# Kernel tuning notes

Hardware: AMD Instinct MI355X
Metric: run time of the kernel (lower is better)

The kernel has to match this reference:

```python
import jax, jax.numpy as jnp
import numpy as np

B, N, IN_DIM = 2, 512, 512
MEM, HID = 300, 64
NEG_SLOPE = 0.01


def setup_inputs() -> dict:
    key = jax.random.key(0)
    ks = jax.random.split(key, 10)
    feature = jax.random.normal(ks[0], (B, N, IN_DIM), dtype=jnp.float32)
    adj = jax.random.randint(ks[1], (B, N, N), 0, 2).astype(jnp.float32)
    s = 0.05
    # per-layer node projections W[l]
    w0 = jax.random.normal(ks[2], (IN_DIM, MEM), dtype=jnp.float32) * s
    b0 = jnp.zeros((MEM,), dtype=jnp.float32)
    w1 = jax.random.normal(ks[3], (MEM, MEM), dtype=jnp.float32) * s
    b1 = jnp.zeros((MEM,), dtype=jnp.float32)
    # shared attention MLP (afcs): Linear(2*MEM, HID) -> ReLU -> Linear(HID, 1)
    a1_w = jax.random.normal(ks[4], (2 * MEM, HID), dtype=jnp.float32) * s
    a1_b = jnp.zeros((HID,), dtype=jnp.float32)
    a2_w = jax.random.normal(ks[5], (HID, 1), dtype=jnp.float32) * s
    a2_b = jnp.zeros((1,), dtype=jnp.float32)
    return {"feature": feature, "adj": adj, "w0": w0, "b0": b0, "w1": w1,
            "b1": b1, "a1_w": a1_w, "a1_b": a1_b, "a2_w": a2_w, "a2_b": a2_b}


def _gat_layer(h_in, adj, w, b, a1_w, a1_b, a2_w, a2_b):
    h = h_in @ w + b                                   # (B,N,M)
    # cat([h_i, h_j]) @ a1_w split into the two halves (same math, no N^2*2M tensor)
    s_i = h @ a1_w[:MEM]                               # (B,N,H)
    s_j = h @ a1_w[MEM:]                               # (B,N,H)
    z = jax.nn.relu(s_i[:, :, None, :] + s_j[:, None, :, :] + a1_b)   # (B,N,N,H)
    e = (z @ a2_w)[..., 0] + a2_b[0]                   # (B,N,N)
    e = jax.nn.leaky_relu(e, negative_slope=NEG_SLOPE)
    b_, n_ = adj.shape[0], adj.shape[1]
    dmask = adj.reshape(b_, n_ * n_)
    logits = e.reshape(b_, n_ * n_) * dmask + (1.0 - dmask) * (-1e30)
    # NOTE: softmax over ALL N*N flattened edges (faithful to original dim=1)
    att = jax.nn.softmax(logits, axis=1).reshape(b_, n_, n_)
    return jnp.einsum('bij,bjd->bid', att, h)


def reference(feature, adj, w0, b0, w1, b1, a1_w, a1_b, a2_w, a2_b):
    f = _gat_layer(feature, adj, w0, b0, a1_w, a1_b, a2_w, a2_b)
    f = _gat_layer(f, adj, w1, b1, a1_w, a1_b, a2_w, a2_b)  # dropout = identity (eval)
    return f
```

## Files before the change

kernel.cpp:

```cpp
#include <hip/hip_runtime.h>

namespace {

constexpr int B_  = 2;
constexpr int N_  = 512;
constexpr int IN_ = 512;
constexpr int M_  = 300;
constexpr int H_  = 64;
constexpr float SLOPE_ = 0.01f;

constexpr long OFF_W0AI = 0;
constexpr long OFF_W0AJ = OFF_W0AI + 512L * 64;
constexpr long OFF_W1AI = OFF_W0AJ + 512L * 64;
constexpr long OFF_W1AJ = OFF_W1AI + 300L * 64;
constexpr long OFF_BSI0 = OFF_W1AJ + 300L * 64;
constexpr long OFF_BSJ0 = OFF_BSI0 + 64;
constexpr long OFF_BSI1 = OFF_BSJ0 + 64;
constexpr long OFF_BSJ1 = OFF_BSI1 + 64;
constexpr long OFF_H0   = OFF_BSJ1 + 64;
constexpr long OFF_H0P  = OFF_H0   + 307200;
constexpr long OFF_SI0P = OFF_H0P  + 2L * 307200;
constexpr long OFF_SJ0P = OFF_SI0P + 4L * 65536;
constexpr long OFF_F1P  = OFF_SJ0P + 4L * 65536;
constexpr long OFF_H1   = OFF_F1P  + 4L * 307200;
constexpr long OFF_H1P  = OFF_H1   + 307200;
constexpr long OFF_SI1P = OFF_H1P  + 2L * 307200;
constexpr long OFF_SJ1P = OFF_SI1P + 2L * 65536;
constexpr long OFF_ZP0  = OFF_SJ1P + 2L * 65536;
constexpr long OFF_ZP1  = OFF_ZP0  + 512;
constexpr long OFF_P0   = OFF_ZP1  + 512;
constexpr long OFF_P1   = OFF_P0   + 2L * 512 * 512;

__device__ __forceinline__ float4 f4add(float4 a, float4 b) {
    a.x += b.x; a.y += b.y; a.z += b.z; a.w += b.w; return a;
}

template<int AFOLD>
__device__ __forceinline__ void gemm_tile(
    const float* __restrict__ A, long afstride,
    const float* __restrict__ W, const float* __restrict__ bias,
    const float* __restrict__ Zp, float* __restrict__ C, long cslice,
    int K, int lda, int Cc, int R, int split, int local,
    float (*As)[38], float (*Ws)[64], float* zred)
{
    const int tx  = (Cc + 63) >> 6;
    const int ty  = (R + 31) >> 5;
    const int nrc = tx * ty;
    const int tile  = local % nrc;
    const int slice = local / nrc;
    const int row0 = (tile / tx) * 32;
    const int col0 = (tile % tx) * 64;
    const int nslab = (K + 31) >> 5;
    const int spl   = (nslab + split - 1) / split;
    const int kb    = slice * spl * 32;
    const int Ke    = min(K, kb + spl * 32);
    C += (long)slice * cslice;

    const int t   = threadIdx.x;
    const int ar  = t >> 3;
    const int ak  = (t & 7) * 4;
    const int arow = min(row0 + ar, R - 1);
    const int wk  = t >> 4;
    const int wc  = (t & 15) * 4;
    const int tm0 = (t >> 4) * 2;
    const int tn0 = (t & 15) * 4;

    auto loadA = [&](int k0) -> float4 {
        const int k = k0 + ak;
        const long base = (long)arow * lda + k;
        float4 r = make_float4(0.f, 0.f, 0.f, 0.f);
        if (k + 3 < Ke) {
            #pragma unroll
            for (int s = 0; s < AFOLD; ++s)
                r = f4add(r, *(const float4*)(A + (long)s * afstride + base));
        } else {
            #pragma unroll
            for (int u = 0; u < 4; ++u)
                if (k + u < Ke) {
                    float v = 0.f;
                    #pragma unroll
                    for (int s = 0; s < AFOLD; ++s)
                        v += A[(long)s * afstride + base + u];
                    (&r.x)[u] = v;
                }
        }
        return r;
    };
    auto loadW = [&](int k0, int s) -> float4 {
        const int gk = k0 + wk + 16 * s;
        if (gk < Ke) {
            const int c = col0 + wc;
            if (c + 3 < Cc) return *(const float4*)(W + (long)gk * Cc + c);
            float tv[4];
            #pragma unroll
            for (int u = 0; u < 4; ++u)
                tv[u] = (c + u < Cc) ? W[(long)gk * Cc + c + u] : 0.0f;
            return make_float4(tv[0], tv[1], tv[2], tv[3]);
        }
        return make_float4(0.f, 0.f, 0.f, 0.f);
    };

    float acc[2][4] = {};
    float4 av  = loadA(kb);
    float4 wv0 = loadW(kb, 0);
    float4 wv1 = loadW(kb, 1);

    for (int k0 = kb; k0 < Ke; k0 += 32) {
        As[ak + 0][ar] = av.x;
        As[ak + 1][ar] = av.y;
        As[ak + 2][ar] = av.z;
        As[ak + 3][ar] = av.w;
        *(float4*)&Ws[wk][wc]      = wv0;
        *(float4*)&Ws[wk + 16][wc] = wv1;
        __syncthreads();

        if (k0 + 32 < Ke) {
            av  = loadA(k0 + 32);
            wv0 = loadW(k0 + 32, 0);
            wv1 = loadW(k0 + 32, 1);
        }

        #pragma unroll
        for (int k = 0; k < 32; ++k) {
            const float a0 = As[k][tm0];
            const float a1 = As[k][tm0 + 1];
            const float4 w4 = *(const float4*)&Ws[k][tn0];
            acc[0][0] = fmaf(a0, w4.x, acc[0][0]);
            acc[0][1] = fmaf(a0, w4.y, acc[0][1]);
            acc[0][2] = fmaf(a0, w4.z, acc[0][2]);
            acc[0][3] = fmaf(a0, w4.w, acc[0][3]);
            acc[1][0] = fmaf(a1, w4.x, acc[1][0]);
            acc[1][1] = fmaf(a1, w4.y, acc[1][1]);
            acc[1][2] = fmaf(a1, w4.z, acc[1][2]);
            acc[1][3] = fmaf(a1, w4.w, acc[1][3]);
        }
        __syncthreads();
    }

    float scale = 1.0f;
    if (Zp != nullptr) {
        float v = Zp[t];
        #pragma unroll
        for (int off = 32; off > 0; off >>= 1)
            v += __shfl_down(v, off, 64);
        if ((t & 63) == 0) zred[t >> 6] = v;
        __syncthreads();
        scale = 1.0f / (zred[0] + zred[1] + zred[2] + zred[3]);
    }

    const int cbase = col0 + tn0;
    float bv[4] = {0.f, 0.f, 0.f, 0.f};
    if (bias != nullptr && slice == 0) {
        #pragma unroll
        for (int u = 0; u < 4; ++u)
            if (cbase + u < Cc) bv[u] = bias[cbase + u];
    }
    #pragma unroll
    for (int i = 0; i < 2; ++i) {
        const int r = row0 + tm0 + i;
        if (r < R) {
            if (cbase + 3 < Cc) {
                float4 o;
                o.x = fmaf(acc[i][0], scale, bv[0]);
                o.y = fmaf(acc[i][1], scale, bv[1]);
                o.z = fmaf(acc[i][2], scale, bv[2]);
                o.w = fmaf(acc[i][3], scale, bv[3]);
                *(float4*)(C + (long)r * Cc + cbase) = o;
            } else {
                #pragma unroll
                for (int u = 0; u < 4; ++u)
                    if (cbase + u < Cc)
                        C[(long)r * Cc + cbase + u] = fmaf(acc[i][u], scale, bv[u]);
            }
        }
    }
}

struct JobsK {
    const float* A[8]; long afstride[8];
    const float* W[8]; const float* bias[8]; const float* Zp[8];
    float* C[8]; long cslice[8];
    int K[8]; int lda[8]; int Cc[8]; int R[8]; int split[8];
    int off[8]; int njobs;
};

template<int AFOLD>
__global__ __launch_bounds__(256)
void gemm_jobs(JobsK jb)
{
    __shared__ __align__(16) float As[32][38];
    __shared__ __align__(16) float Ws[32][64];
    __shared__ float zred[4];

    const int bid = blockIdx.x;
    int j = jb.njobs - 1;
    while (j > 0 && bid < jb.off[j]) --j;
    const int local = bid - jb.off[j];

    gemm_tile<AFOLD>(jb.A[j], jb.afstride[j], jb.W[j], jb.bias[j], jb.Zp[j],
                     jb.C[j], jb.cslice[j], jb.K[j], jb.lda[j], jb.Cc[j],
                     jb.R[j], jb.split[j], local, As, Ws, zred);
}

template<int FOLD>
__device__ __forceinline__ void attn_tile(
    const float* __restrict__ si, const float* __restrict__ sj, long fstride,
    const float* __restrict__ adj, const float* __restrict__ a2w,
    const float* __restrict__ a2b, float* __restrict__ p,
    float* __restrict__ Zpart, int g,
    float (*Si)[68], float (*Sj)[68], float* red)
{
    const int b    = g >> 8;
    const int tile = g & 255;
    const int i0 = (tile >> 4) * 32;
    const int j0 = (tile & 15) * 32;
    const int t  = threadIdx.x;

    {
        const int r  = t >> 3;
        const int hc = (t & 7) * 8;
        const long gib = ((long)(b * N_ + i0 + r)) * H_ + hc;
        const long gjb = ((long)(b * N_ + j0 + r)) * H_ + hc;
        float4 a0 = make_float4(0.f, 0.f, 0.f, 0.f);
        float4 a1 = a0, b0v = a0, b1v = a0;
        #pragma unroll
        for (int s = 0; s < FOLD; ++s) {
            const float* gi = si + (long)s * fstride + gib;
            const float* gj = sj + (long)s * fstride + gjb;
            a0  = f4add(a0,  *(const float4*)(gi));
            a1  = f4add(a1,  *(const float4*)(gi + 4));
            b0v = f4add(b0v, *(const float4*)(gj));
            b1v = f4add(b1v, *(const float4*)(gj + 4));
        }
        *(float4*)&Si[r][hc]     = a0;
        *(float4*)&Si[r][hc + 4] = a1;
        *(float4*)&Sj[r][hc]     = b0v;
        *(float4*)&Sj[r][hc + 4] = b1v;
    }
    __syncthreads();

    const int i  = t >> 3;
    const int jl = t & 7;

    float e[4] = {0.f, 0.f, 0.f, 0.f};
    #pragma unroll
    for (int h0 = 0; h0 < H_; h0 += 4) {
        const float4 a4 = *(const float4*)&Si[i][h0];
        const float w0v = a2w[h0 + 0];
        const float w1v = a2w[h0 + 1];
        const float w2v = a2w[h0 + 2];
        const float w3v = a2w[h0 + 3];
        #pragma unroll
        for (int u = 0; u < 4; ++u) {
            const float4 b4 = *(const float4*)&Sj[jl + 8 * u][h0];
            e[u] = fmaf(fmaxf(a4.x + b4.x, 0.f), w0v, e[u]);
            e[u] = fmaf(fmaxf(a4.y + b4.y, 0.f), w1v, e[u]);
            e[u] = fmaf(fmaxf(a4.z + b4.z, 0.f), w2v, e[u]);
            e[u] = fmaf(fmaxf(a4.w + b4.w, 0.f), w3v, e[u]);
        }
    }

    const float a2bv = a2b[0];
    const long rowbase = ((long)(b * N_ + i0 + i)) * N_ + j0 + jl;
    float lsum = 0.f;
    #pragma unroll
    for (int u = 0; u < 4; ++u) {
        float ev = e[u] + a2bv;
        ev = (ev >= 0.f) ? ev : SLOPE_ * ev;
        const float m  = adj[rowbase + 8 * u];
        const float pv = m * __expf(ev);
        p[rowbase + 8 * u] = pv;
        lsum += pv;
    }

    #pragma unroll
    for (int off = 32; off > 0; off >>= 1)
        lsum += __shfl_down(lsum, off, 64);
    if ((t & 63) == 0) red[t >> 6] = lsum;
    __syncthreads();
    if (t == 0)
        Zpart[b * 256 + tile] = red[0] + red[1] + red[2] + red[3];
}

template<int FOLD>
__global__ __launch_bounds__(256)
void attn_fused(const float* __restrict__ si, const float* __restrict__ sj,
                const float* __restrict__ adj, const float* __restrict__ a2w,
                const float* __restrict__ a2b, float* __restrict__ p,
                float* __restrict__ Zpart,
                const float4* __restrict__ hsrc, float4* __restrict__ hdst)
{
    __shared__ __align__(16) float Si[32][68];
    __shared__ __align__(16) float Sj[32][68];
    __shared__ float red[4];

    const int bx = blockIdx.x;
    if (bx < 512) {
        attn_tile<FOLD>(si, sj, 65536, adj, a2w, a2b, p, Zpart, bx,
                        Si, Sj, red);
    } else {
        const int tid = (bx - 512) * 256 + threadIdx.x;
        for (int i = tid; i < 76800; i += 65536)
            hdst[i] = f4add(hsrc[i], hsrc[i + 76800]);
    }
}

}

extern "C" void kernel_launch(void* const* d_in, const int* in_sizes, int n_in,
                              void* d_out, int out_size, void* d_ws, size_t ws_size,
                              hipStream_t stream)
{
    (void)in_sizes; (void)n_in; (void)out_size; (void)ws_size;
    const float* feature = (const float*)d_in[0];
    const float* adj     = (const float*)d_in[1];
    const float* w0      = (const float*)d_in[2];
    const float* b0      = (const float*)d_in[3];
    const float* w1      = (const float*)d_in[4];
    const float* b1      = (const float*)d_in[5];
    const float* a1w     = (const float*)d_in[6];
    const float* a1b     = (const float*)d_in[7];
    const float* a2w     = (const float*)d_in[8];
    const float* a2b     = (const float*)d_in[9];
    float* out = (float*)d_out;
    float* ws  = (float*)d_ws;

    float* cW0Ai = ws + OFF_W0AI;
    float* cW0Aj = ws + OFF_W0AJ;
    float* cW1Ai = ws + OFF_W1AI;
    float* cW1Aj = ws + OFF_W1AJ;
    float* bsi0  = ws + OFF_BSI0;
    float* bsj0  = ws + OFF_BSJ0;
    float* bsi1  = ws + OFF_BSI1;
    float* bsj1  = ws + OFF_BSJ1;
    float* h0    = ws + OFF_H0;
    float* h0p   = ws + OFF_H0P;
    float* si0p  = ws + OFF_SI0P;
    float* sj0p  = ws + OFF_SJ0P;
    float* f1p   = ws + OFF_F1P;
    float* h1    = ws + OFF_H1;
    float* h1p   = ws + OFF_H1P;
    float* si1p  = ws + OFF_SI1P;
    float* sj1p  = ws + OFF_SJ1P;
    float* Zp0   = ws + OFF_ZP0;
    float* Zp1   = ws + OFF_ZP1;
    float* p0    = ws + OFF_P0;
    float* p1    = ws + OFF_P1;

    const float* Ai = a1w;
    const float* Aj = a1w + (long)M_ * H_;

    auto set_job = [](JobsK& jb, int j, const float* A, long afstride,
                      const float* W, const float* bias, const float* Zp,
                      float* C, long cslice, int K, int lda, int Cc, int R,
                      int split, int& tiles) {
        jb.A[j] = A; jb.afstride[j] = afstride;
        jb.W[j] = W; jb.bias[j] = bias; jb.Zp[j] = Zp;
        jb.C[j] = C; jb.cslice[j] = cslice;
        jb.K[j] = K; jb.lda[j] = lda; jb.Cc[j] = Cc; jb.R[j] = R;
        jb.split[j] = split;
        jb.off[j] = tiles;
        tiles += ((R + 31) / 32) * ((Cc + 63) / 64) * split;
    };

    {
        JobsK jb; int tiles = 0;
        set_job(jb, 0, w0, 0, Ai, nullptr, nullptr, cW0Ai, 0, M_, M_, H_, IN_, 1, tiles);
        set_job(jb, 1, w0, 0, Aj, nullptr, nullptr, cW0Aj, 0, M_, M_, H_, IN_, 1, tiles);
        set_job(jb, 2, w1, 0, Ai, nullptr, nullptr, cW1Ai, 0, M_, M_, H_, M_,  1, tiles);
        set_job(jb, 3, w1, 0, Aj, nullptr, nullptr, cW1Aj, 0, M_, M_, H_, M_,  1, tiles);
        set_job(jb, 4, b0, 0, Ai, nullptr, nullptr, bsi0,  0, M_, M_, H_, 1,   1, tiles);
        set_job(jb, 5, b0, 0, Aj, a1b,     nullptr, bsj0,  0, M_, M_, H_, 1,   1, tiles);
        set_job(jb, 6, b1, 0, Ai, nullptr, nullptr, bsi1,  0, M_, M_, H_, 1,   1, tiles);
        set_job(jb, 7, b1, 0, Aj, a1b,     nullptr, bsj1,  0, M_, M_, H_, 1,   1, tiles);
        jb.njobs = 8;
        gemm_jobs<1><<<dim3(tiles), dim3(256), 0, stream>>>(jb);
    }

    {
        JobsK jb; int tiles = 0;
        set_job(jb, 0, feature, 0, w0,    b0,   nullptr, h0p,  307200,
                IN_, IN_, M_, 1024, 2, tiles);
        set_job(jb, 1, feature, 0, cW0Ai, bsi0, nullptr, si0p, 65536,
                IN_, IN_, H_, 1024, 4, tiles);
        set_job(jb, 2, feature, 0, cW0Aj, bsj0, nullptr, sj0p, 65536,
                IN_, IN_, H_, 1024, 4, tiles);
        jb.njobs = 3;
        gemm_jobs<1><<<dim3(tiles), dim3(256), 0, stream>>>(jb);
    }

    attn_fused<4><<<dim3(768), dim3(256), 0, stream>>>(
        si0p, sj0p, adj, a2w, a2b, p0, Zp0, (const float4*)h0p, (float4*)h0);

    {
        JobsK jb; int tiles = 0;
        set_job(jb, 0, p0, 0, h0, nullptr, Zp0, f1p, 307200,
                N_, N_, M_, N_, 4, tiles);
        set_job(jb, 1, p0 + (long)N_*N_, 0, h0 + (long)N_*M_, nullptr,
                Zp0 + 256, f1p + (long)N_*M_, 307200,
                N_, N_, M_, N_, 4, tiles);
        jb.njobs = 2;
        gemm_jobs<1><<<dim3(tiles), dim3(256), 0, stream>>>(jb);
    }

    {
        JobsK jb; int tiles = 0;
        set_job(jb, 0, f1p, 307200, w1,    b1,   nullptr, h1p,  307200,
                M_, M_, M_, 1024, 2, tiles);
        set_job(jb, 1, f1p, 307200, cW1Ai, bsi1, nullptr, si1p, 65536,
                M_, M_, H_, 1024, 2, tiles);
        set_job(jb, 2, f1p, 307200, cW1Aj, bsj1, nullptr, sj1p, 65536,
                M_, M_, H_, 1024, 2, tiles);
        jb.njobs = 3;
        gemm_jobs<4><<<dim3(tiles), dim3(256), 0, stream>>>(jb);
    }

    attn_fused<2><<<dim3(768), dim3(256), 0, stream>>>(
        si1p, sj1p, adj, a2w, a2b, p1, Zp1, (const float4*)h1p, (float4*)h1);

    {
        JobsK jb; int tiles = 0;
        set_job(jb, 0, p1, 0, h1, nullptr, Zp1, out, 0,
                N_, N_, M_, N_, 1, tiles);
        set_job(jb, 1, p1 + (long)N_*N_, 0, h1 + (long)N_*M_, nullptr,
                Zp1 + 256, out + (long)N_*M_, 0,
                N_, N_, M_, N_, 1, tiles);
        jb.njobs = 2;
        gemm_jobs<1><<<dim3(tiles), dim3(256), 0, stream>>>(jb);
    }
}
```

Baseline: 174.6 us.

## Use 64x64 register-blocked GEMM tiles and restructure layer-0 projection pipeline

The GEMM kernel now has templated block sizes: 64x64 tiles with a 4x4 per-thread micro-tile, swizzled shared-memory A storage, and a 64-thread 32x32 variant for the final aggregation. Layer 0 now computes h0 first and derives s_i/s_j from h0 instead of from precomposed W0·A matrices. Split-K partial sums are folded on load in both A and W operands, which removes the separate h-reduction blocks in the attention kernel. The aim is higher arithmetic intensity per shared load and less redundant work. The cost is an extra dependent launch in layer 0 and a different split and occupancy balance.

```diff
diff --git a/kernel.cpp b/kernel.cpp
--- a/kernel.cpp
+++ b/kernel.cpp
@@ -9,146 +9,198 @@
 constexpr int H_  = 64;
 constexpr float SLOPE_ = 0.01f;
 
-constexpr long OFF_W0AI = 0;
-constexpr long OFF_W0AJ = OFF_W0AI + 512L * 64;
-constexpr long OFF_W1AI = OFF_W0AJ + 512L * 64;
-constexpr long OFF_W1AJ = OFF_W1AI + 300L * 64;
-constexpr long OFF_BSI0 = OFF_W1AJ + 300L * 64;
-constexpr long OFF_BSJ0 = OFF_BSI0 + 64;
-constexpr long OFF_BSI1 = OFF_BSJ0 + 64;
-constexpr long OFF_BSJ1 = OFF_BSI1 + 64;
-constexpr long OFF_H0   = OFF_BSJ1 + 64;
-constexpr long OFF_H0P  = OFF_H0   + 307200;
-constexpr long OFF_SI0P = OFF_H0P  + 2L * 307200;
-constexpr long OFF_SJ0P = OFF_SI0P + 4L * 65536;
-constexpr long OFF_F1P  = OFF_SJ0P + 4L * 65536;
-constexpr long OFF_H1   = OFF_F1P  + 4L * 307200;
-constexpr long OFF_H1P  = OFF_H1   + 307200;
-constexpr long OFF_SI1P = OFF_H1P  + 2L * 307200;
-constexpr long OFF_SJ1P = OFF_SI1P + 2L * 65536;
-constexpr long OFF_ZP0  = OFF_SJ1P + 2L * 65536;
-constexpr long OFF_ZP1  = OFF_ZP0  + 512;
-constexpr long OFF_P0   = OFF_ZP1  + 512;
-constexpr long OFF_P1   = OFF_P0   + 2L * 512 * 512;
+constexpr long OFF_CW1AI = 0;
+constexpr long OFF_CW1AJ = OFF_CW1AI + 19200;
+constexpr long OFF_BS1I  = OFF_CW1AJ + 19200;
+constexpr long OFF_BS1J  = OFF_BS1I  + 64;
+constexpr long OFF_H0S   = OFF_BS1J  + 64;
+constexpr long OFF_SI0S  = OFF_H0S   + 3L * 307200;
+constexpr long OFF_SJ0S  = OFF_SI0S  + 4L * 65536;
+constexpr long OFF_F1S   = OFF_SJ0S  + 4L * 65536;
+constexpr long OFF_H1S   = OFF_F1S   + 3L * 307200;
+constexpr long OFF_SI1S  = OFF_H1S   + 2L * 307200;
+constexpr long OFF_SJ1S  = OFF_SI1S  + 2L * 65536;
+constexpr long OFF_ZP0   = OFF_SJ1S  + 2L * 65536;
+constexpr long OFF_ZP1   = OFF_ZP0   + 512;
+constexpr long OFF_P0    = OFF_ZP1   + 512;
+constexpr long OFF_P1    = OFF_P0    + 524288;
 
 __device__ __forceinline__ float4 f4add(float4 a, float4 b) {
     a.x += b.x; a.y += b.y; a.z += b.z; a.w += b.w; return a;
 }
 
-template<int AFOLD>
-__device__ __forceinline__ void gemm_tile(
-    const float* __restrict__ A, long afstride,
-    const float* __restrict__ W, const float* __restrict__ bias,
-    const float* __restrict__ Zp, float* __restrict__ C, long cslice,
-    int K, int lda, int Cc, int R, int split, int local,
-    float (*As)[38], float (*Ws)[64], float* zred)
+struct JobsK {
+    const float* A[5]; long afs[5];
+    const float* W[5]; long wfs[5];
+    const float* bias[5]; const float* Zp[5];
+    float* C[5]; long cslice[5];
+    int K[5]; int lda[5]; int Cc[5]; int R[5]; int split[5];
+    int off[5]; int njobs;
+};
+
+template<int TPB, int AFOLD, int WFOLD>
+__global__ __launch_bounds__(TPB)
+void gemm_jobs(JobsK jb)
 {
-    const int tx  = (Cc + 63) >> 6;
-    const int ty  = (R + 31) >> 5;
+    constexpr int TM  = (TPB == 256) ? 64 : 32;
+    constexpr int TN  = TM;
+    constexpr int APT = 32 * TM / TPB;
+    constexpr int AQW = 32 / APT;
+    constexpr int WQW = TPB / 32;
+    constexpr int WPT = TN / WQW;
+    constexpr int TCW = TN / 4;
+
+    __shared__ __align__(16) float As[32][TM + 4];
+    __shared__ __align__(16) float Ws[32][TN + 4];
+    __shared__ float zred[4];
+
+    const int bid = blockIdx.x;
+    int j = jb.njobs - 1;
+    while (j > 0 && bid < jb.off[j]) --j;
+    const int local = bid - jb.off[j];
+
+    const float* __restrict__ A = jb.A[j];  const long afs = jb.afs[j];
+    const float* __restrict__ W = jb.W[j];  const long wfs = jb.wfs[j];
+    const float* bias = jb.bias[j];
+    const float* Zp   = jb.Zp[j];
+    float* __restrict__ C = jb.C[j];
+    const int K = jb.K[j], lda = jb.lda[j], Cc = jb.Cc[j], R = jb.R[j];
+    const int split = jb.split[j];
+
+    const int tx  = (Cc + TN - 1) / TN;
+    const int ty  = (R + TM - 1) / TM;
     const int nrc = tx * ty;
     const int tile  = local % nrc;
     const int slice = local / nrc;
-    const int row0 = (tile / tx) * 32;
-    const int col0 = (tile % tx) * 64;
+    const int row0 = (tile / tx) * TM;
+    const int col0 = (tile % tx) * TN;
     const int nslab = (K + 31) >> 5;
     const int spl   = (nslab + split - 1) / split;
     const int kb    = slice * spl * 32;
     const int Ke    = min(K, kb + spl * 32);
-    C += (long)slice * cslice;
-
-    const int t   = threadIdx.x;
-    const int ar  = t >> 3;
-    const int ak  = (t & 7) * 4;
+    C += (long)slice * jb.cslice[j];
+
+    const int t  = threadIdx.x;
+    const int ar = t / AQW, aq = t % AQW;
     const int arow = min(row0 + ar, R - 1);
-    const int wk  = t >> 4;
-    const int wc  = (t & 15) * 4;
-    const int tm0 = (t >> 4) * 2;
-    const int tn0 = (t & 15) * 4;
-
-    auto loadA = [&](int k0) -> float4 {
-        const int k = k0 + ak;
-        const long base = (long)arow * lda + k;
-        float4 r = make_float4(0.f, 0.f, 0.f, 0.f);
-        if (k + 3 < Ke) {
+    const int wr = t / WQW, wq = t % WQW;
+    const int tr = t / TCW, tc = t % TCW;
+
+    float4 av[APT / 4], wv[WPT / 4];
+
+    auto loadA = [&](int k0) {
+        #pragma unroll
+        for (int f = 0; f < APT / 4; ++f) {
+            const int k = k0 + aq * APT + f * 4;
+            const long base = (long)arow * lda + k;
+            float4 r = make_float4(0.f, 0.f, 0.f, 0.f);
+            if (k + 3 < Ke) {
+                #pragma unroll
+                for (int s = 0; s < AFOLD; ++s)
+                    r = f4add(r, *(const float4*)(A + (long)s * afs + base));
+            } else {
+                #pragma unroll
+                for (int u = 0; u < 4; ++u)
+                    if (k + u < Ke) {
+                        float v = 0.f;
+                        #pragma unroll
+                        for (int s = 0; s < AFOLD; ++s)
+                            v += A[(long)s * afs + base + u];
+                        (&r.x)[u] = v;
+                    }
+            }
+            av[f] = r;
+        }
+    };
+    auto loadW = [&](int k0) {
+        const int gk = k0 + wr;
+        #pragma unroll
+        for (int f = 0; f < WPT / 4; ++f) {
+            const int c = col0 + wq * WPT + f * 4;
+            float4 r = make_float4(0.f, 0.f, 0.f, 0.f);
+            if (gk < Ke) {
+                const long base = (long)gk * Cc + c;
+                if (c + 3 < Cc) {
+                    #pragma unroll
+                    for (int s = 0; s < WFOLD; ++s)
+                        r = f4add(r, *(const float4*)(W + (long)s * wfs + base));
+                } else {
+                    #pragma unroll
+                    for (int u = 0; u < 4; ++u)
+                        if (c + u < Cc) {
+                            float v = 0.f;
+                            #pragma unroll
+                            for (int s = 0; s < WFOLD; ++s)
+                                v += W[(long)s * wfs + base + u];
+                            (&r.x)[u] = v;
+                        }
+                }
+            }
+            wv[f] = r;
+        }
+    };
+
+    float acc[4][4] = {};
+    loadA(kb);
+    loadW(kb);
+
+    for (int k0 = kb; k0 < Ke; k0 += 32) {
+        #pragma unroll
+        for (int f = 0; f < APT / 4; ++f) {
             #pragma unroll
-            for (int s = 0; s < AFOLD; ++s)
-                r = f4add(r, *(const float4*)(A + (long)s * afstride + base));
-        } else {
+            for (int c = 0; c < 4; ++c) {
+                const int kk = aq * APT + f * 4 + c;
+                const int s  = (kk >> 3) & 3;
+                As[kk][ar ^ (s << 2)] = (&av[f].x)[c];
+            }
+        }
+        #pragma unroll
+        for (int f = 0; f < WPT / 4; ++f)
+            *(float4*)&Ws[wr][wq * WPT + 4 * f] = wv[f];
+        __syncthreads();
+
+        if (k0 + 32 < Ke) {
+            loadA(k0 + 32);
+            loadW(k0 + 32);
+        }
+
+        #pragma unroll
+        for (int k = 0; k < 32; ++k) {
+            const int s = (k >> 3) & 3;
+            const float4 a4 = *(const float4*)&As[k][(tr ^ s) * 4];
+            const float4 w4 = *(const float4*)&Ws[k][tc * 4];
+            const float a_[4] = {a4.x, a4.y, a4.z, a4.w};
             #pragma unroll
-            for (int u = 0; u < 4; ++u)
-                if (k + u < Ke) {
-                    float v = 0.f;
-                    #pragma unroll
-                    for (int s = 0; s < AFOLD; ++s)
-                        v += A[(long)s * afstride + base + u];
-                    (&r.x)[u] = v;
-                }
-        }
-        return r;
-    };
-    auto loadW = [&](int k0, int s) -> float4 {
-        const int gk = k0 + wk + 16 * s;
-        if (gk < Ke) {
-            const int c = col0 + wc;
-            if (c + 3 < Cc) return *(const float4*)(W + (long)gk * Cc + c);
-            float tv[4];
-            #pragma unroll
-            for (int u = 0; u < 4; ++u)
-                tv[u] = (c + u < Cc) ? W[(long)gk * Cc + c + u] : 0.0f;
-            return make_float4(tv[0], tv[1], tv[2], tv[3]);
-        }
-        return make_float4(0.f, 0.f, 0.f, 0.f);
-    };
-
-    float acc[2][4] = {};
-    float4 av  = loadA(kb);
-    float4 wv0 = loadW(kb, 0);
-    float4 wv1 = loadW(kb, 1);
-
-    for (int k0 = kb; k0 < Ke; k0 += 32) {
-        As[ak + 0][ar] = av.x;
-        As[ak + 1][ar] = av.y;
-        As[ak + 2][ar] = av.z;
-        As[ak + 3][ar] = av.w;
-        *(float4*)&Ws[wk][wc]      = wv0;
-        *(float4*)&Ws[wk + 16][wc] = wv1;
-        __syncthreads();
-
-        if (k0 + 32 < Ke) {
-            av  = loadA(k0 + 32);
-            wv0 = loadW(k0 + 32, 0);
-            wv1 = loadW(k0 + 32, 1);
-        }
-
-        #pragma unroll
-        for (int k = 0; k < 32; ++k) {
-            const float a0 = As[k][tm0];
-            const float a1 = As[k][tm0 + 1];
-            const float4 w4 = *(const float4*)&Ws[k][tn0];
-            acc[0][0] = fmaf(a0, w4.x, acc[0][0]);
-            acc[0][1] = fmaf(a0, w4.y, acc[0][1]);
-            acc[0][2] = fmaf(a0, w4.z, acc[0][2]);
-            acc[0][3] = fmaf(a0, w4.w, acc[0][3]);
-            acc[1][0] = fmaf(a1, w4.x, acc[1][0]);
-            acc[1][1] = fmaf(a1, w4.y, acc[1][1]);
-            acc[1][2] = fmaf(a1, w4.z, acc[1][2]);
-            acc[1][3] = fmaf(a1, w4.w, acc[1][3]);
+            for (int i = 0; i < 4; ++i) {
+                acc[i][0] = fmaf(a_[i], w4.x, acc[i][0]);
+                acc[i][1] = fmaf(a_[i], w4.y, acc[i][1]);
+                acc[i][2] = fmaf(a_[i], w4.z, acc[i][2]);
+                acc[i][3] = fmaf(a_[i], w4.w, acc[i][3]);
+            }
         }
         __syncthreads();
     }
 
     float scale = 1.0f;
     if (Zp != nullptr) {
-        float v = Zp[t];
-        #pragma unroll
-        for (int off = 32; off > 0; off >>= 1)
-            v += __shfl_down(v, off, 64);
-        if ((t & 63) == 0) zred[t >> 6] = v;
-        __syncthreads();
-        scale = 1.0f / (zred[0] + zred[1] + zred[2] + zred[3]);
-    }
-
-    const int cbase = col0 + tn0;
+        if constexpr (TPB == 256) {
+            float v = Zp[t];
+            #pragma unroll
+            for (int off = 32; off > 0; off >>= 1)
+                v += __shfl_down(v, off, 64);
+            if ((t & 63) == 0) zred[t >> 6] = v;
+            __syncthreads();
+            scale = 1.0f / (zred[0] + zred[1] + zred[2] + zred[3]);
+        } else {
+            float v = Zp[t] + Zp[t + 64] + Zp[t + 128] + Zp[t + 192];
+            #pragma unroll
+            for (int off = 32; off > 0; off >>= 1)
+                v += __shfl_down(v, off, 64);
+            scale = 1.0f / __shfl(v, 0, 64);
+        }
+    }
+
+    const int cbase = col0 + tc * 4;
     float bv[4] = {0.f, 0.f, 0.f, 0.f};
     if (bias != nullptr && slice == 0) {
         #pragma unroll
@@ -156,8 +208,8 @@
             if (cbase + u < Cc) bv[u] = bias[cbase + u];
     }
     #pragma unroll
-    for (int i = 0; i < 2; ++i) {
-        const int r = row0 + tm0 + i;
+    for (int i = 0; i < 4; ++i) {
+        const int r = row0 + tr * 4 + i;
         if (r < R) {
             if (cbase + 3 < Cc) {
                 float4 o;
@@ -176,40 +228,18 @@
     }
 }
 
-struct JobsK {
-    const float* A[8]; long afstride[8];
-    const float* W[8]; const float* bias[8]; const float* Zp[8];
-    float* C[8]; long cslice[8];
-    int K[8]; int lda[8]; int Cc[8]; int R[8]; int split[8];
-    int off[8]; int njobs;
-};
-
-template<int AFOLD>
+template<int FOLD>
 __global__ __launch_bounds__(256)
-void gemm_jobs(JobsK jb)
+void attn_k(const float* __restrict__ si, const float* __restrict__ sj,
+            const float* __restrict__ adj, const float* __restrict__ a2w,
+            const float* __restrict__ a2b, float* __restrict__ p,
+            float* __restrict__ Zpart)
 {
-    __shared__ __align__(16) float As[32][38];
-    __shared__ __align__(16) float Ws[32][64];
-    __shared__ float zred[4];
-
-    const int bid = blockIdx.x;
-    int j = jb.njobs - 1;
-    while (j > 0 && bid < jb.off[j]) --j;
-    const int local = bid - jb.off[j];
-
-    gemm_tile<AFOLD>(jb.A[j], jb.afstride[j], jb.W[j], jb.bias[j], jb.Zp[j],
-                     jb.C[j], jb.cslice[j], jb.K[j], jb.lda[j], jb.Cc[j],
-                     jb.R[j], jb.split[j], local, As, Ws, zred);
-}
-
-template<int FOLD>
-__device__ __forceinline__ void attn_tile(
-    const float* __restrict__ si, const float* __restrict__ sj, long fstride,
-    const float* __restrict__ adj, const float* __restrict__ a2w,
-    const float* __restrict__ a2b, float* __restrict__ p,
-    float* __restrict__ Zpart, int g,
-    float (*Si)[68], float (*Sj)[68], float* red)
-{
+    __shared__ __align__(16) float Si[32][68];
+    __shared__ __align__(16) float Sj[32][68];
+    __shared__ float red[4];
+
+    const int g    = blockIdx.x;
     const int b    = g >> 8;
     const int tile = g & 255;
     const int i0 = (tile >> 4) * 32;
@@ -225,8 +255,8 @@
         float4 a1 = a0, b0v = a0, b1v = a0;
         #pragma unroll
         for (int s = 0; s < FOLD; ++s) {
-            const float* gi = si + (long)s * fstride + gib;
-            const float* gj = sj + (long)s * fstride + gjb;
+            const float* gi = si + (long)s * 65536 + gib;
+            const float* gj = sj + (long)s * 65536 + gjb;
             a0  = f4add(a0,  *(const float4*)(gi));
             a1  = f4add(a1,  *(const float4*)(gi + 4));
             b0v = f4add(b0v, *(const float4*)(gj));
@@ -280,29 +310,6 @@
     __syncthreads();
     if (t == 0)
         Zpart[b * 256 + tile] = red[0] + red[1] + red[2] + red[3];
-}
-
-template<int FOLD>
-__global__ __launch_bounds__(256)
-void attn_fused(const float* __restrict__ si, const float* __restrict__ sj,
-                const float* __restrict__ adj, const float* __restrict__ a2w,
-                const float* __restrict__ a2b, float* __restrict__ p,
-                float* __restrict__ Zpart,
-                const float4* __restrict__ hsrc, float4* __restrict__ hdst)
-{
-    __shared__ __align__(16) float Si[32][68];
-    __shared__ __align__(16) float Sj[32][68];
-    __shared__ float red[4];
-
-    const int bx = blockIdx.x;
-    if (bx < 512) {
-        attn_tile<FOLD>(si, sj, 65536, adj, a2w, a2b, p, Zpart, bx,
-                        Si, Sj, red);
-    } else {
-        const int tid = (bx - 512) * 256 + threadIdx.x;
-        for (int i = tid; i < 76800; i += 65536)
-            hdst[i] = f4add(hsrc[i], hsrc[i + 76800]);
-    }
 }
 
 }
@@ -325,23 +332,17 @@
     float* out = (float*)d_out;
     float* ws  = (float*)d_ws;
 
-    float* cW0Ai = ws + OFF_W0AI;
-    float* cW0Aj = ws + OFF_W0AJ;
-    float* cW1Ai = ws + OFF_W1AI;
-    float* cW1Aj = ws + OFF_W1AJ;
-    float* bsi0  = ws + OFF_BSI0;
-    float* bsj0  = ws + OFF_BSJ0;
-    float* bsi1  = ws + OFF_BSI1;
-    float* bsj1  = ws + OFF_BSJ1;
-    float* h0    = ws + OFF_H0;
-    float* h0p   = ws + OFF_H0P;
-    float* si0p  = ws + OFF_SI0P;
-    float* sj0p  = ws + OFF_SJ0P;
-    float* f1p   = ws + OFF_F1P;
-    float* h1    = ws + OFF_H1;
-    float* h1p   = ws + OFF_H1P;
-    float* si1p  = ws + OFF_SI1P;
-    float* sj1p  = ws + OFF_SJ1P;
+    float* cW1Ai = ws + OFF_CW1AI;
+    float* cW1Aj = ws + OFF_CW1AJ;
+    float* bs1i  = ws + OFF_BS1I;
+    float* bs1j  = ws + OFF_BS1J;
+    float* h0s   = ws + OFF_H0S;
+    float* si0s  = ws + OFF_SI0S;
+    float* sj0s  = ws + OFF_SJ0S;
+    float* f1s   = ws + OFF_F1S;
+    float* h1s   = ws + OFF_H1S;
+    float* si1s  = ws + OFF_SI1S;
+    float* sj1s  = ws + OFF_SJ1S;
     float* Zp0   = ws + OFF_ZP0;
     float* Zp1   = ws + OFF_ZP1;
     float* p0    = ws + OFF_P0;
@@ -350,82 +351,84 @@
     const float* Ai = a1w;
     const float* Aj = a1w + (long)M_ * H_;
 
-    auto set_job = [](JobsK& jb, int j, const float* A, long afstride,
-                      const float* W, const float* bias, const float* Zp,
-                      float* C, long cslice, int K, int lda, int Cc, int R,
-                      int split, int& tiles) {
-        jb.A[j] = A; jb.afstride[j] = afstride;
-        jb.W[j] = W; jb.bias[j] = bias; jb.Zp[j] = Zp;
+    auto set_job = [](JobsK& jb, int j, const float* A, long afs,
+                      const float* W, long wfs, const float* bias,
+                      const float* Zp, float* C, long cslice,
+                      int K, int lda, int Cc, int R, int split,
+                      int TM, int& tiles) {
+        jb.A[j] = A; jb.afs[j] = afs;
+        jb.W[j] = W; jb.wfs[j] = wfs;
+        jb.bias[j] = bias; jb.Zp[j] = Zp;
         jb.C[j] = C; jb.cslice[j] = cslice;
         jb.K[j] = K; jb.lda[j] = lda; jb.Cc[j] = Cc; jb.R[j] = R;
         jb.split[j] = split;
         jb.off[j] = tiles;
-        tiles += ((R + 31) / 32) * ((Cc + 63) / 64) * split;
+        tiles += ((R + TM - 1) / TM) * ((Cc + TM - 1) / TM) * split;
     };
 
     {
         JobsK jb; int tiles = 0;
-        set_job(jb, 0, w0, 0, Ai, nullptr, nullptr, cW0Ai, 0, M_, M_, H_, IN_, 1, tiles);
-        set_job(jb, 1, w0, 0, Aj, nullptr, nullptr, cW0Aj, 0, M_, M_, H_, IN_, 1, tiles);
-        set_job(jb, 2, w1, 0, Ai, nullptr, nullptr, cW1Ai, 0, M_, M_, H_, M_,  1, tiles);
-        set_job(jb, 3, w1, 0, Aj, nullptr, nullptr, cW1Aj, 0, M_, M_, H_, M_,  1, tiles);
-        set_job(jb, 4, b0, 0, Ai, nullptr, nullptr, bsi0,  0, M_, M_, H_, 1,   1, tiles);
-        set_job(jb, 5, b0, 0, Aj, a1b,     nullptr, bsj0,  0, M_, M_, H_, 1,   1, tiles);
-        set_job(jb, 6, b1, 0, Ai, nullptr, nullptr, bsi1,  0, M_, M_, H_, 1,   1, tiles);
-        set_job(jb, 7, b1, 0, Aj, a1b,     nullptr, bsj1,  0, M_, M_, H_, 1,   1, tiles);
-        jb.njobs = 8;
-        gemm_jobs<1><<<dim3(tiles), dim3(256), 0, stream>>>(jb);
+        set_job(jb, 0, feature, 0, w0, 0, b0, nullptr, h0s, 307200,
+                IN_, IN_, M_, 1024, 3, 64, tiles);
+        set_job(jb, 1, w1, 0, Ai, 0, nullptr, nullptr, cW1Ai, 0,
+                M_, M_, H_, M_, 1, 64, tiles);
+        set_job(jb, 2, w1, 0, Aj, 0, nullptr, nullptr, cW1Aj, 0,
+                M_, M_, H_, M_, 1, 64, tiles);
+        set_job(jb, 3, b1, 0, Ai, 0, nullptr, nullptr, bs1i, 0,
+                M_, M_, H_, 1, 1, 64, tiles);
+        set_job(jb, 4, b1, 0, Aj, 0, a1b, nullptr, bs1j, 0,
+                M_, M_, H_, 1, 1, 64, tiles);
+        jb.njobs = 5;
+        gemm_jobs<256, 1, 1><<<dim3(tiles), dim3(256), 0, stream>>>(jb);
     }
 
     {
         JobsK jb; int tiles = 0;
-        set_job(jb, 0, feature, 0, w0,    b0,   nullptr, h0p,  307200,
-                IN_, IN_, M_, 1024, 2, tiles);
-        set_job(jb, 1, feature, 0, cW0Ai, bsi0, nullptr, si0p, 65536,
-                IN_, IN_, H_, 1024, 4, tiles);
-        set_job(jb, 2, feature, 0, cW0Aj, bsj0, nullptr, sj0p, 65536,
-                IN_, IN_, H_, 1024, 4, tiles);
+        set_job(jb, 0, h0s, 307200, Ai, 0, nullptr, nullptr, si0s, 65536,
+                M_, M_, H_, 1024, 4, 64, tiles);
+        set_job(jb, 1, h0s, 307200, Aj, 0, a1b, nullptr, sj0s, 65536,
+                M_, M_, H_, 1024, 4, 64, tiles);
+        jb.njobs = 2;
+        gemm_jobs<256, 3, 1><<<dim3(tiles), dim3(256), 0, stream>>>(jb);
+    }
+
+    attn_k<4><<<dim3(512), dim3(256), 0, stream>>>(
+        si0s, sj0s, adj, a2w, a2b, p0, Zp0);
+
+    {
+        JobsK jb; int tiles = 0;
+        set_job(jb, 0, p0, 0, h0s, 307200, nullptr, Zp0, f1s, 307200,
+                N_, N_, M_, N_, 3, 64, tiles);
+        set_job(jb, 1, p0 + 262144, 0, h0s + 153600, 307200, nullptr,
+                Zp0 + 256, f1s + 153600, 307200,
+                N_, N_, M_, N_, 3, 64, tiles);
+        jb.njobs = 2;
+        gemm_jobs<256, 1, 3><<<dim3(tiles), dim3(256), 0, stream>>>(jb);
+    }
+
+    {
+        JobsK jb; int tiles = 0;
+        set_job(jb, 0, f1s, 307200, w1, 0, b1, nullptr, h1s, 307200,
+                M_, M_, M_, 1024, 2, 64, tiles);
+        set_job(jb, 1, f1s, 307200, cW1Ai, 0, bs1i, nullptr, si1s, 65536,
+                M_, M_, H_, 1024, 2, 64, tiles);
+        set_job(jb, 2, f1s, 307200, cW1Aj, 0, bs1j, nullptr, sj1s, 65536,
+                M_, M_, H_, 1024, 2, 64, tiles);
         jb.njobs = 3;
-        gemm_jobs<1><<<dim3(tiles), dim3(256), 0, stream>>>(jb);
-    }
-
-    attn_fused<4><<<dim3(768), dim3(256), 0, stream>>>(
-        si0p, sj0p, adj, a2w, a2b, p0, Zp0, (const float4*)h0p, (float4*)h0);
+        gemm_jobs<256, 3, 1><<<dim3(tiles), dim3(256), 0, stream>>>(jb);
+    }
+
+    attn_k<2><<<dim3(512), dim3(256), 0, stream>>>(
+        si1s, sj1s, adj, a2w, a2b, p1, Zp1);
 
     {
         JobsK jb; int tiles = 0;
-        set_job(jb, 0, p0, 0, h0, nullptr, Zp0, f1p, 307200,
-                N_, N_, M_, N_, 4, tiles);
-        set_job(jb, 1, p0 + (long)N_*N_, 0, h0 + (long)N_*M_, nullptr,
-                Zp0 + 256, f1p + (long)N_*M_, 307200,
-                N_, N_, M_, N_, 4, tiles);
+        set_job(jb, 0, p1, 0, h1s, 307200, nullptr, Zp1, out, 0,
+                N_, N_, M_, N_, 1, 32, tiles);
+        set_job(jb, 1, p1 + 262144, 0, h1s + 153600, 307200, nullptr,
+                Zp1 + 256, out + 153600, 0,
+                N_, N_, M_, N_, 1, 32, tiles);
         jb.njobs = 2;
-        gemm_jobs<1><<<dim3(tiles), dim3(256), 0, stream>>>(jb);
-    }
-
-    {
-        JobsK jb; int tiles = 0;
-        set_job(jb, 0, f1p, 307200, w1,    b1,   nullptr, h1p,  307200,
-                M_, M_, M_, 1024, 2, tiles);
-        set_job(jb, 1, f1p, 307200, cW1Ai, bsi1, nullptr, si1p, 65536,
-                M_, M_, H_, 1024, 2, tiles);
-        set_job(jb, 2, f1p, 307200, cW1Aj, bsj1, nullptr, sj1p, 65536,
-                M_, M_, H_, 1024, 2, tiles);
-        jb.njobs = 3;
-        gemm_jobs<4><<<dim3(tiles), dim3(256), 0, stream>>>(jb);
-    }
-
-    attn_fused<2><<<dim3(768), dim3(256), 0, stream>>>(
-        si1p, sj1p, adj, a2w, a2b, p1, Zp1, (const float4*)h1p, (float4*)h1);
-
-    {
-        JobsK jb; int tiles = 0;
-        set_job(jb, 0, p1, 0, h1, nullptr, Zp1, out, 0,
-                N_, N_, M_, N_, 1, tiles);
-        set_job(jb, 1, p1 + (long)N_*N_, 0, h1 + (long)N_*M_, nullptr,
-                Zp1 + 256, out + (long)N_*M_, 0,
-                N_, N_, M_, N_, 1, tiles);
-        jb.njobs = 2;
-        gemm_jobs<1><<<dim3(tiles), dim3(256), 0, stream>>>(jb);
+        gemm_jobs<64, 1, 2><<<dim3(tiles), dim3(64), 0, stream>>>(jb);
     }
 }
```

New measurement: 211.1 us. 20.9% more time.
